# Optimization experiments

Hardware: AMD Instinct MI355X
Metric: run time of the kernel (lower is better)

The kernel has to match this reference:

```python
import jax, jax.numpy as jnp
import numpy as np

B, H, W, BLK = 32, 512, 512, 8
QF_MIN, QF_MAX, QF_BIAS = 2.0, 50.0, 0.0

_RGB2YCC = jnp.array([[0.299, 0.587, 0.114],
                      [-0.168736, -0.331264, 0.5],
                      [0.5, -0.418688, -0.081312]], jnp.float32)
_YCC_OFF = jnp.array([0.0, 128.0, 128.0], jnp.float32)

Y_QTB = jnp.array([16,11,10,16,24,40,51,61,12,12,14,19,26,58,60,55,14,13,16,24,40,57,69,56,
                   14,17,22,29,51,87,80,62,18,22,37,56,68,109,103,77,24,36,55,64,81,104,113,92,
                   49,64,78,87,103,121,120,101,72,92,95,98,112,100,103,99], jnp.float32).reshape(8, 8)
C_QTB = jnp.array([17,18,24,47,99,99,99,99,18,21,26,66,99,99,99,99,24,26,56,99,99,99,99,99,
                   47,66,99,99,99,99,99,99,99,99,99,99,99,99,99,99,99,99,99,99,99,99,99,99,
                   99,99,99,99,99,99,99,99,99,99,99,99,99,99,99,99], jnp.float32).reshape(8, 8)

# orthonormal 8x8 DCT-II matrix
_k = np.arange(8.0)[:, None]; _n = np.arange(8.0)[None, :]
_C = 0.5 * np.cos((2 * _n + 1) * _k * np.pi / 16.0)
_C[0] *= 1.0 / np.sqrt(2.0)
DCT_M = jnp.asarray(_C, jnp.float32)

# standard JPEG zig-zag raster order over the 64 coefficients of an 8x8 block
ZIGZAG = jnp.array([0,1,8,16,9,2,3,10,17,24,32,25,18,11,4,5,12,19,26,33,40,48,41,34,27,20,13,6,
                    7,14,21,28,35,42,49,56,57,50,43,36,29,22,15,23,30,37,44,51,58,59,52,45,38,31,
                    39,46,53,60,61,54,47,55,62,63], jnp.int32)


def hard_round(x):
    # straight-through round: forward = round(x), backward = identity
    return x + jax.lax.stop_gradient(jnp.round(x) - x)


def split_blocks(x):
    # [B,H,W] -> [B,H/8,W/8,8,8]
    b, h, w = x.shape
    return x.reshape(b, h // BLK, BLK, w // BLK, BLK).transpose(0, 1, 3, 2, 4)


def dct2d(x):
    # 2D DCT over the trailing 8x8 dims: C @ X @ C^T
    return jnp.einsum('ij,bnmjk,lk->bnmil', DCT_M, x, DCT_M)


def _norm01(e):
    mn = e.min(axis=(1, 2), keepdims=True)
    mx = e.max(axis=(1, 2), keepdims=True)
    return (e - mn) / (mx - mn + 1e-6)


def _ac_energy(d):
    # per-block log AC energy, shape [B,h8,w8]
    return jnp.log1p(jnp.sum(d * d, axis=(-2, -1)) - d[..., 0, 0] ** 2 + 1e-6)


def _forward(rgb):
    ycbcr = hard_round(jnp.einsum('bhwc,kc->bhwk', rgb, _RGB2YCC) + _YCC_OFF) - 128.0
    y_d = dct2d(split_blocks(ycbcr[..., 0]))
    cb_d = dct2d(split_blocks(ycbcr[..., 1]))
    cr_d = dct2d(split_blocks(ycbcr[..., 2]))

    # QFMapGenerator (default): per-block AC-energy rank in [0,1], upsampled to pixels
    rank = jnp.stack([_norm01(_ac_energy(y_d)),
                      _norm01(0.5 * (_ac_energy(cb_d) + _ac_energy(cr_d)))], axis=-1)  # [B,h8,w8,2]
    rank_px = jnp.repeat(jnp.repeat(rank, BLK, axis=1), BLK, axis=2)  # [B,H,W,2]

    # RankToQF
    enc_qf = jnp.clip(hard_round(QF_MIN + rank_px * (QF_MAX - QF_MIN) + QF_BIAS), QF_MIN, QF_MAX)
    y_qf_min = enc_qf[..., 0].min(axis=(1, 2), keepdims=True)
    y_qf_max = enc_qf[..., 0].max(axis=(1, 2), keepdims=True)
    c_qf_min = enc_qf[..., 1].min(axis=(1, 2), keepdims=True)
    c_qf_max = enc_qf[..., 1].max(axis=(1, 2), keepdims=True)

    # QFToScale: standard JPEG QF -> scale factor
    enc_scale = hard_round(jnp.where(enc_qf < 50.0, 5000.0 / enc_qf, 200.0 - 2.0 * enc_qf)) / 100.0

    sy = split_blocks(enc_scale[..., 0])  # [B,h8,w8,8,8]
    sc = split_blocks(enc_scale[..., 1])
    yq = hard_round(y_d / (sy * Y_QTB))
    cbq = hard_round(cb_d / (sc * C_QTB))
    crq = hard_round(cr_d / (sc * C_QTB))
    qdct = jnp.stack([yq, cbq, crq], axis=1)  # [B,3,h8,w8,8,8]

    nb = (H // BLK) * (W // BLK)
    flat = qdct.reshape(B, 3, nb, 64)
    # delta encode along the block axis
    delta = jnp.concatenate([flat[:, :, :1], flat[:, :, 1:] - flat[:, :, :-1]], axis=2)
    # zig-zag raster scan of the 64 coefficients
    zz = delta[..., ZIGZAG]
    blocks = jnp.log(jnp.abs(zz) + 1.0) / jnp.log(2.0)
    blocks = blocks.reshape(-1, 64)
    return qdct, blocks, enc_qf, enc_scale, y_qf_min, y_qf_max, c_qf_min, c_qf_max


def setup_inputs() -> dict:
    key = jax.random.key(0)
    rgb = jax.random.uniform(key, (B, H, W, 3), jnp.float32) * 255.0
    return {"rgb": rgb}


def reference(rgb):
    return _forward(rgb)
```

## Files before the change

kernel.cpp:

```cpp
#include <hip/hip_runtime.h>
#include <math.h>

#define BB 32
#define HH 512
#define WW 512
#define NB 4096
#define QD 25165824
#define PP 16777216
#define TAILOFF (2 * (size_t)QD + 2 * (size_t)PP)

__constant__ int c_zz[64] = {
    0,1,8,16,9,2,3,10,17,24,32,25,18,11,4,5,12,19,26,33,40,48,41,34,27,20,13,6,
    7,14,21,28,35,42,49,56,57,50,43,36,29,22,15,23,30,37,44,51,58,59,52,45,38,31,
    39,46,53,60,61,54,47,55,62,63};

struct QArg { float Cf[64]; double rqY[64]; double rqC[64]; };

__device__ __forceinline__ double qf_from_rank(double r) {
    double q = rint(2.0 + r * 48.0 + 0.0);
    return fmin(fmax(q, 2.0), 50.0);
}
__device__ __forceinline__ double scale_from_qf(double qf) {
    double s = (qf < 50.0) ? (5000.0 / qf) : (200.0 - 2.0 * qf);
    return rint(s) / 100.0;
}

__device__ __forceinline__ void ycc16(const float* __restrict__ src, int p0,
                                      int* y, int* cb, int* cr) {
    float px[48];
    const float4* s4 = (const float4*)(src + (size_t)p0 * 3);
    #pragma unroll
    for (int k = 0; k < 12; ++k) ((float4*)px)[k] = s4[k];
    #pragma unroll
    for (int k = 0; k < 16; ++k) {
        double R = px[3 * k], G = px[3 * k + 1], Bv = px[3 * k + 2];
        y[k]  = (int)(rint(R * (double)0.299f     + G * (double)0.587f     + Bv * (double)0.114f)             - 128.0);
        cb[k] = (int)(rint(R * (double)-0.168736f + G * (double)-0.331264f + Bv * (double)0.5f       + 128.0) - 128.0);
        cr[k] = (int)(rint(R * (double)0.5f       + G * (double)-0.418688f + Bv * (double)-0.081312f + 128.0) - 128.0);
    }
}

__global__ __launch_bounds__(256, 4) void k_energy(const float* __restrict__ rgb,
                                                   short* __restrict__ planes,
                                                   double* __restrict__ ey,
                                                   double* __restrict__ ec) {
    __shared__ int4 part[3][8][32];
    __shared__ double ecomb[2][64];
    int b = blockIdx.x >> 6, i = blockIdx.x & 63, t = threadIdx.x;
    const float* src = rgb + (size_t)(b * HH + i * 8) * WW * 3;
    {
        int y[16], cb[16], cr[16];
        ycc16(src, t * 16, y, cb, cr);
        int s[3][2] = {{0,0},{0,0},{0,0}}, s2[3][2] = {{0,0},{0,0},{0,0}};
        alignas(16) short yb[16], cbb[16], crb[16];
        #pragma unroll
        for (int k = 0; k < 16; ++k) {
            int h = k >> 3;
            s[0][h] += y[k];  s2[0][h] += y[k] * y[k];
            s[1][h] += cb[k]; s2[1][h] += cb[k] * cb[k];
            s[2][h] += cr[k]; s2[2][h] += cr[k] * cr[k];
            yb[k] = (short)y[k]; cbb[k] = (short)cb[k]; crb[k] = (short)cr[k];
        }
        size_t soff = (size_t)i * 4096 + (size_t)t * 16;
        short* d0 = planes + (((size_t)(b * 3 + 0)) << 18) + soff;
        short* d1 = planes + (((size_t)(b * 3 + 1)) << 18) + soff;
        short* d2 = planes + (((size_t)(b * 3 + 2)) << 18) + soff;
        ((int4*)d0)[0] = ((int4*)yb)[0];  ((int4*)d0)[1] = ((int4*)yb)[1];
        ((int4*)d1)[0] = ((int4*)cbb)[0]; ((int4*)d1)[1] = ((int4*)cbb)[1];
        ((int4*)d2)[0] = ((int4*)crb)[0]; ((int4*)d2)[1] = ((int4*)crb)[1];
        int r0 = t >> 5, c = t & 31;
        #pragma unroll
        for (int ch = 0; ch < 3; ++ch)
            part[ch][r0][c] = make_int4(s[ch][0], s2[ch][0], s[ch][1], s2[ch][1]);
    }
    __syncthreads();
    int ch = t >> 6, j = t & 63;
    if (ch < 3) {
        int S = 0, S2 = 0;
        #pragma unroll
        for (int r = 0; r < 8; ++r) {
            const int2* p = (const int2*)&part[ch][r][j >> 1];
            int2 v = p[j & 1];
            S += v.x; S2 += v.y;
        }
        double e = log1p((double)S2 - (double)S * (double)S * (1.0 / 64.0) + 1e-6);
        if (ch == 0) ey[b * NB + i * 64 + j] = e;
        else ecomb[ch - 1][j] = e;
    }
    __syncthreads();
    if (t < 64) ec[b * NB + i * 64 + t] = 0.5 * (ecomb[0][t] + ecomb[1][t]);
}

__global__ __launch_bounds__(256) void k_minmax(const double* __restrict__ ey,
                                                const double* __restrict__ ec,
                                                double* __restrict__ mm,
                                                float* __restrict__ out_tail) {
    __shared__ double s0[256], s1[256], s2[256], s3[256];
    int b = blockIdx.x, tid = threadIdx.x;
    double mny = 1e300, mxy = -1e300, mnc = 1e300, mxc = -1e300;
    for (int n = tid; n < NB; n += 256) {
        double vy = ey[b * NB + n], vc = ec[b * NB + n];
        mny = fmin(mny, vy); mxy = fmax(mxy, vy);
        mnc = fmin(mnc, vc); mxc = fmax(mxc, vc);
    }
    s0[tid] = mny; s1[tid] = mxy; s2[tid] = mnc; s3[tid] = mxc;
    __syncthreads();
    for (int off = 128; off > 0; off >>= 1) {
        if (tid < off) {
            s0[tid] = fmin(s0[tid], s0[tid + off]);
            s1[tid] = fmax(s1[tid], s1[tid + off]);
            s2[tid] = fmin(s2[tid], s2[tid + off]);
            s3[tid] = fmax(s3[tid], s3[tid + off]);
        }
        __syncthreads();
    }
    if (tid == 0) {
        mm[b] = s0[0]; mm[32 + b] = s1[0]; mm[64 + b] = s2[0]; mm[96 + b] = s3[0];
        double ry = (s1[0] - s0[0]) / (s1[0] - s0[0] + 1e-6);
        double rc = (s3[0] - s2[0]) / (s3[0] - s2[0] + 1e-6);
        out_tail[b]      = (float)qf_from_rank(0.0);
        out_tail[32 + b] = (float)qf_from_rank(ry);
        out_tail[64 + b] = (float)qf_from_rank(0.0);
        out_tail[96 + b] = (float)qf_from_rank(rc);
    }
}

__global__ __launch_bounds__(256, 4) void k_quant(const short* __restrict__ planes,
                                                  QArg A,
                                                  const double* __restrict__ ey,
                                                  const double* __restrict__ ec,
                                                  const double* __restrict__ mm,
                                                  float* __restrict__ out) {
    __shared__ __align__(16) char lds[27136];
    short* sqA = (short*)lds;
    float4* qsc = (float4*)(lds + 26112);

    int b = blockIdx.x >> 6, i = blockIdx.x & 63, t = threadIdx.x;
    int ch = t >> 6, j = t & 63;
    float U[8][8];
    double qy = 0, qc = 0, sy = 1, sc = 1;
    if (ch < 3) {
        int gt = b * NB + i * 64 + j;
        double eyv = ey[gt], ecv = ec[gt];
        double mny = mm[b], mxy = mm[32 + b], mnc = mm[64 + b], mxc = mm[96 + b];
        double ry = (eyv - mny) / (mxy - mny + 1e-6);
        double rc = (ecv - mnc) / (mxc - mnc + 1e-6);
        qy = qf_from_rank(ry); qc = qf_from_rank(rc);
        sy = scale_from_qf(qy); sc = scale_from_qf(qc);
        const short* pl = planes + (((size_t)(b * 3 + ch)) << 18)
                        + (size_t)i * 4096 + (size_t)j * 8;
        #pragma unroll
        for (int r = 0; r < 8; ++r) {
            alignas(16) short xs[8];
            *(int4*)xs = *(const int4*)(pl + (size_t)r * 512);
            float xr[8];
            #pragma unroll
            for (int s = 0; s < 8; ++s) xr[s] = (float)xs[s];
            #pragma unroll
            for (int v = 0; v < 8; ++v) {
                float u = 0.0f;
                #pragma unroll
                for (int s = 0; s < 8; ++s) u += xr[s] * A.Cf[v * 8 + s];
                U[r][v] = u;
            }
        }
        if (ch == 0) qsc[j] = make_float4((float)qy, (float)qc, (float)sy, (float)sc);
        double rinv = 1.0 / ((ch == 0) ? sy : sc);
        const double* rqt = (ch == 0) ? A.rqY : A.rqC;
        int row = (ch * 64 + j) * 68;
        #pragma unroll
        for (int u = 0; u < 8; ++u) {
            alignas(8) short srow[8];
            #pragma unroll
            for (int v = 0; v < 8; ++v) {
                float dq = (float)rint([&]{
                    float d = 0.0f;
                    #pragma unroll
                    for (int r = 0; r < 8; ++r) d += A.Cf[u * 8 + r] * U[r][v];
                    return (double)d * (rqt[u * 8 + v] * rinv);
                }());
                srow[v] = (short)(int)dq;
            }
            ((long long*)&sqA[row + u * 8])[0] = ((long long*)srow)[0];
            ((long long*)&sqA[row + u * 8 + 4])[0] = ((long long*)srow)[1];
        }
    }
    __syncthreads();

    size_t obase = ((size_t)b * 3 * NB + (size_t)i * 64) * 64;
    int k4 = (t & 15) * 4;
    #pragma unroll
    for (int it = 0; it < 12; ++it) {
        int m = it * 256 + t;
        int mch = m >> 10, f = m & 1023;
        int mj = f >> 4;
        alignas(8) short s4[4];
        *(long long*)s4 = *(const long long*)&sqA[(mch * 64 + mj) * 68 + k4];
        float4 v = make_float4((float)s4[0], (float)s4[1], (float)s4[2], (float)s4[3]);
        *(float4*)(out + obase + (size_t)mch * NB * 64 + (size_t)mj * 64 + k4) = v;
    }
    int zk0 = c_zz[k4], zk1 = c_zz[k4 + 1], zk2 = c_zz[k4 + 2], zk3 = c_zz[k4 + 3];
    #pragma unroll
    for (int it = 0; it < 12; ++it) {
        int m = it * 256 + t;
        int mch = m >> 10, f = m & 1023;
        int mj = f >> 4;
        int rowc = (mch * 64 + mj) * 68;
        int rowp = rowc - (mj ? 68 : 0);
        float d0 = (float)(sqA[rowc + zk0] - sqA[rowp + zk0]);
        float d1 = (float)(sqA[rowc + zk1] - sqA[rowp + zk1]);
        float d2 = (float)(sqA[rowc + zk2] - sqA[rowp + zk2]);
        float d3 = (float)(sqA[rowc + zk3] - sqA[rowp + zk3]);
        float4 v = make_float4(log2f(fabsf(d0) + 1.0f),
                               log2f(fabsf(d1) + 1.0f),
                               log2f(fabsf(d2) + 1.0f),
                               log2f(fabsf(d3) + 1.0f));
        *(float4*)(out + QD + obase + (size_t)mch * NB * 64 + (size_t)mj * 64 + k4) = v;
    }
    {
        float4 qs = qsc[t >> 2];
        float4 qv = make_float4(qs.x, qs.y, qs.x, qs.y);
        float4 sv = make_float4(qs.z, qs.w, qs.z, qs.w);
        float2* mq = (float2*)(out + 2 * (size_t)QD);
        float2* ms = (float2*)(out + 2 * (size_t)QD + PP);
        #pragma unroll
        for (int rr = 0; rr < 8; ++rr) {
            size_t P = ((size_t)(b * HH + i * 8 + rr)) * WW;
            ((float4*)(mq + P))[t] = qv;
            ((float4*)(ms + P))[t] = sv;
        }
    }
}

__global__ __launch_bounds__(256) void k_fix(const float* __restrict__ q,
                                             float* __restrict__ ob) {
    int idx = blockIdx.x * 256 + threadIdx.x;
    int rid = idx >> 6, k = idx & 63;
    int bch = rid >> 6;
    int i = rid & 63;
    size_t base = ((size_t)bch * NB + (size_t)i * 64) * 64;
    int zk = c_zz[k];
    float cur = q[base + zk];
    float prv = (i > 0) ? q[base - 64 + zk] : 0.0f;
    ob[base + k] = log2f(fabsf(cur - prv) + 1.0f);
}

extern "C" void kernel_launch(void* const* d_in, const int* in_sizes, int n_in,
                              void* d_out, int out_size, void* d_ws, size_t ws_size,
                              hipStream_t stream) {
    const float* rgb = (const float*)d_in[0];
    float* out = (float*)d_out;
    double* ws = (double*)d_ws;
    double* ey = ws;
    double* ec = ws + (size_t)BB * NB;
    double* mm = ws + 2 * (size_t)BB * NB;
    short* planes = (short*)(ws + 2 * (size_t)BB * NB + 128);

    static const double YQ[64] = {
        16,11,10,16,24,40,51,61, 12,12,14,19,26,58,60,55, 14,13,16,24,40,57,69,56,
        14,17,22,29,51,87,80,62, 18,22,37,56,68,109,103,77, 24,36,55,64,81,104,113,92,
        49,64,78,87,103,121,120,101, 72,92,95,98,112,100,103,99};
    static const double CQ[64] = {
        17,18,24,47,99,99,99,99, 18,21,26,66,99,99,99,99, 24,26,56,99,99,99,99,99,
        47,66,99,99,99,99,99,99, 99,99,99,99,99,99,99,99, 99,99,99,99,99,99,99,99,
        99,99,99,99,99,99,99,99, 99,99,99,99,99,99,99,99};

    QArg qa;
    for (int k = 0; k < 8; ++k)
        for (int n = 0; n < 8; ++n) {
            double v = 0.5 * cos((2.0 * n + 1.0) * (double)k * M_PI / 16.0);
            if (k == 0) v *= 0.70710678118654752440;
            qa.Cf[k * 8 + n] = (float)v;
        }
    for (int k = 0; k < 64; ++k) { qa.rqY[k] = 1.0 / YQ[k]; qa.rqC[k] = 1.0 / CQ[k]; }

    dim3 blk(256);
    k_energy<<<BB * 64, blk, 0, stream>>>(rgb, planes, ey, ec);
    k_minmax<<<BB, blk, 0, stream>>>(ey, ec, mm, out + TAILOFF);
    k_quant<<<BB * 64, blk, 0, stream>>>(planes, qa, ey, ec, mm, out);
    k_fix<<<(BB * 3 * 64 * 64) / 256, blk, 0, stream>>>(out, out + QD);
}
```

Baseline: 435.3 us.

## Fuse min/max reduction and cross-row delta fixup into quantization kernel

Removes the separate per-image min/max kernel: every quant block now redundantly reduces the image's 4096 energy values itself. It also drops the fixup kernel, which re-read the quantized output to redo the delta at row boundaries. Three extra threads now recompute the last block of the previous row into shared memory so the delta can be finished in-block. This cuts two launches and a large global read/write pass, at the cost of redundant reduction reads (64 blocks per image) and extra DCT work for three threads.

```diff
diff --git a/kernel.cpp b/kernel.cpp
--- a/kernel.cpp
+++ b/kernel.cpp
@@ -91,64 +91,71 @@
     if (t < 64) ec[b * NB + i * 64 + t] = 0.5 * (ecomb[0][t] + ecomb[1][t]);
 }
 
-__global__ __launch_bounds__(256) void k_minmax(const double* __restrict__ ey,
-                                                const double* __restrict__ ec,
-                                                double* __restrict__ mm,
-                                                float* __restrict__ out_tail) {
-    __shared__ double s0[256], s1[256], s2[256], s3[256];
-    int b = blockIdx.x, tid = threadIdx.x;
-    double mny = 1e300, mxy = -1e300, mnc = 1e300, mxc = -1e300;
-    for (int n = tid; n < NB; n += 256) {
-        double vy = ey[b * NB + n], vc = ec[b * NB + n];
-        mny = fmin(mny, vy); mxy = fmax(mxy, vy);
-        mnc = fmin(mnc, vc); mxc = fmax(mxc, vc);
-    }
-    s0[tid] = mny; s1[tid] = mxy; s2[tid] = mnc; s3[tid] = mxc;
-    __syncthreads();
-    for (int off = 128; off > 0; off >>= 1) {
-        if (tid < off) {
-            s0[tid] = fmin(s0[tid], s0[tid + off]);
-            s1[tid] = fmax(s1[tid], s1[tid + off]);
-            s2[tid] = fmin(s2[tid], s2[tid + off]);
-            s3[tid] = fmax(s3[tid], s3[tid + off]);
-        }
-        __syncthreads();
-    }
-    if (tid == 0) {
-        mm[b] = s0[0]; mm[32 + b] = s1[0]; mm[64 + b] = s2[0]; mm[96 + b] = s3[0];
-        double ry = (s1[0] - s0[0]) / (s1[0] - s0[0] + 1e-6);
-        double rc = (s3[0] - s2[0]) / (s3[0] - s2[0] + 1e-6);
-        out_tail[b]      = (float)qf_from_rank(0.0);
-        out_tail[32 + b] = (float)qf_from_rank(ry);
-        out_tail[64 + b] = (float)qf_from_rank(0.0);
-        out_tail[96 + b] = (float)qf_from_rank(rc);
-    }
-}
-
 __global__ __launch_bounds__(256, 4) void k_quant(const short* __restrict__ planes,
                                                   QArg A,
                                                   const double* __restrict__ ey,
                                                   const double* __restrict__ ec,
-                                                  const double* __restrict__ mm,
                                                   float* __restrict__ out) {
-    __shared__ __align__(16) char lds[27136];
+    __shared__ __align__(16) char lds[27584];
     short* sqA = (short*)lds;
-    float4* qsc = (float4*)(lds + 26112);
+    float4* qsc = (float4*)(lds + 26560);
+    double* red = (double*)lds;
 
     int b = blockIdx.x >> 6, i = blockIdx.x & 63, t = threadIdx.x;
-    int ch = t >> 6, j = t & 63;
-    float U[8][8];
-    double qy = 0, qc = 0, sy = 1, sc = 1;
-    if (ch < 3) {
-        int gt = b * NB + i * 64 + j;
+
+    double mny = 1e300, mxy = -1e300, mnc = 1e300, mxc = -1e300;
+    const double* eyb = ey + (size_t)b * NB;
+    const double* ecb = ec + (size_t)b * NB;
+    for (int n = t; n < NB; n += 256) {
+        double vy = eyb[n], vc = ecb[n];
+        mny = fmin(mny, vy); mxy = fmax(mxy, vy);
+        mnc = fmin(mnc, vc); mxc = fmax(mxc, vc);
+    }
+    red[t] = mny; red[256 + t] = mxy; red[512 + t] = mnc; red[768 + t] = mxc;
+    __syncthreads();
+    for (int off = 128; off > 0; off >>= 1) {
+        if (t < off) {
+            red[t]       = fmin(red[t],       red[t + off]);
+            red[256 + t] = fmax(red[256 + t], red[256 + t + off]);
+            red[512 + t] = fmin(red[512 + t], red[512 + t + off]);
+            red[768 + t] = fmax(red[768 + t], red[768 + t + off]);
+        }
+        __syncthreads();
+    }
+    mny = red[0]; mxy = red[256]; mnc = red[512]; mxc = red[768];
+    __syncthreads();
+
+    if (i == 0 && t == 0) {
+        double ry = (mxy - mny) / (mxy - mny + 1e-6);
+        double rc = (mxc - mnc) / (mxc - mnc + 1e-6);
+        float* tail = out + TAILOFF;
+        tail[b]      = (float)qf_from_rank(0.0);
+        tail[32 + b] = (float)qf_from_rank(ry);
+        tail[64 + b] = (float)qf_from_rank(0.0);
+        tail[96 + b] = (float)qf_from_rank(rc);
+    }
+
+    int ch = 0, j = 0, ii = i, row = 0;
+    bool act = false, zero = false;
+    if (t < 192)      { ch = t >> 6;  j = t & 63; row = (ch * 64 + j) * 68; act = true; }
+    else if (t < 195) { ch = t - 192; j = 63; ii = i - 1; row = (192 + ch) * 68;
+                        act = true; zero = (i == 0); }
+
+    if (act && zero) {
+        #pragma unroll
+        for (int u = 0; u < 16; ++u) ((long long*)&sqA[row])[u] = 0LL;
+    }
+    if (act && !zero) {
+        int gt = b * NB + ii * 64 + j;
         double eyv = ey[gt], ecv = ec[gt];
-        double mny = mm[b], mxy = mm[32 + b], mnc = mm[64 + b], mxc = mm[96 + b];
         double ry = (eyv - mny) / (mxy - mny + 1e-6);
         double rc = (ecv - mnc) / (mxc - mnc + 1e-6);
-        qy = qf_from_rank(ry); qc = qf_from_rank(rc);
-        sy = scale_from_qf(qy); sc = scale_from_qf(qc);
+        double qy = qf_from_rank(ry), qc = qf_from_rank(rc);
+        double sy = scale_from_qf(qy), sc = scale_from_qf(qc);
+        if (t < 64) qsc[j] = make_float4((float)qy, (float)qc, (float)sy, (float)sc);
         const short* pl = planes + (((size_t)(b * 3 + ch)) << 18)
-                        + (size_t)i * 4096 + (size_t)j * 8;
+                        + (size_t)ii * 4096 + (size_t)j * 8;
+        float U[8][8];
         #pragma unroll
         for (int r = 0; r < 8; ++r) {
             alignas(16) short xs[8];
@@ -164,10 +171,8 @@
                 U[r][v] = u;
             }
         }
-        if (ch == 0) qsc[j] = make_float4((float)qy, (float)qc, (float)sy, (float)sc);
         double rinv = 1.0 / ((ch == 0) ? sy : sc);
         const double* rqt = (ch == 0) ? A.rqY : A.rqC;
-        int row = (ch * 64 + j) * 68;
         #pragma unroll
         for (int u = 0; u < 8; ++u) {
             alignas(8) short srow[8];
@@ -206,7 +211,7 @@
         int mch = m >> 10, f = m & 1023;
         int mj = f >> 4;
         int rowc = (mch * 64 + mj) * 68;
-        int rowp = rowc - (mj ? 68 : 0);
+        int rowp = mj ? (rowc - 68) : (192 + mch) * 68;
         float d0 = (float)(sqA[rowc + zk0] - sqA[rowp + zk0]);
         float d1 = (float)(sqA[rowc + zk1] - sqA[rowp + zk1]);
         float d2 = (float)(sqA[rowc + zk2] - sqA[rowp + zk2]);
@@ -232,19 +237,6 @@
     }
 }
 
-__global__ __launch_bounds__(256) void k_fix(const float* __restrict__ q,
-                                             float* __restrict__ ob) {
-    int idx = blockIdx.x * 256 + threadIdx.x;
-    int rid = idx >> 6, k = idx & 63;
-    int bch = rid >> 6;
-    int i = rid & 63;
-    size_t base = ((size_t)bch * NB + (size_t)i * 64) * 64;
-    int zk = c_zz[k];
-    float cur = q[base + zk];
-    float prv = (i > 0) ? q[base - 64 + zk] : 0.0f;
-    ob[base + k] = log2f(fabsf(cur - prv) + 1.0f);
-}
-
 extern "C" void kernel_launch(void* const* d_in, const int* in_sizes, int n_in,
                               void* d_out, int out_size, void* d_ws, size_t ws_size,
                               hipStream_t stream) {
@@ -253,8 +245,7 @@
     double* ws = (double*)d_ws;
     double* ey = ws;
     double* ec = ws + (size_t)BB * NB;
-    double* mm = ws + 2 * (size_t)BB * NB;
-    short* planes = (short*)(ws + 2 * (size_t)BB * NB + 128);
+    short* planes = (short*)(ws + 2 * (size_t)BB * NB);
 
     static const double YQ[64] = {
         16,11,10,16,24,40,51,61, 12,12,14,19,26,58,60,55, 14,13,16,24,40,57,69,56,
@@ -276,7 +267,5 @@
 
     dim3 blk(256);
     k_energy<<<BB * 64, blk, 0, stream>>>(rgb, planes, ey, ec);
-    k_minmax<<<BB, blk, 0, stream>>>(ey, ec, mm, out + TAILOFF);
-    k_quant<<<BB * 64, blk, 0, stream>>>(planes, qa, ey, ec, mm, out);
-    k_fix<<<(BB * 3 * 64 * 64) / 256, blk, 0, stream>>>(out, out + QD);
-}
+    k_quant<<<BB * 64, blk, 0, stream>>>(planes, qa, ey, ec, out);
+}
```

After: 445.0 us. 1.02x slower.

## Store YCbCr planes as int8 and fold boundary delta fix into quant kernel

Applied to the files above, without the earlier changes.

The intermediate YCbCr planes are stored as signed 8-bit values instead of 16-bit shorts, halving the bytes written by the energy kernel and read by the quant kernel. The separate k_fix launch, which recomputed zig-zag deltas for the first block of each block-row, is removed. Instead, three extra threads in k_quant recompute the quantized last block of the previous row into LDS so the delta for j=0 is correct in place. This adds redundant DCT work for one block per channel per workgroup and depends on every rounded YCbCr value fitting in int8.

```diff
diff --git a/kernel.cpp b/kernel.cpp
--- a/kernel.cpp
+++ b/kernel.cpp
@@ -41,7 +41,7 @@
 }
 
 __global__ __launch_bounds__(256, 4) void k_energy(const float* __restrict__ rgb,
-                                                   short* __restrict__ planes,
+                                                   signed char* __restrict__ planes,
                                                    double* __restrict__ ey,
                                                    double* __restrict__ ec) {
     __shared__ int4 part[3][8][32];
@@ -52,22 +52,22 @@
         int y[16], cb[16], cr[16];
         ycc16(src, t * 16, y, cb, cr);
         int s[3][2] = {{0,0},{0,0},{0,0}}, s2[3][2] = {{0,0},{0,0},{0,0}};
-        alignas(16) short yb[16], cbb[16], crb[16];
+        alignas(16) signed char yb[16], cbb[16], crb[16];
         #pragma unroll
         for (int k = 0; k < 16; ++k) {
             int h = k >> 3;
             s[0][h] += y[k];  s2[0][h] += y[k] * y[k];
             s[1][h] += cb[k]; s2[1][h] += cb[k] * cb[k];
             s[2][h] += cr[k]; s2[2][h] += cr[k] * cr[k];
-            yb[k] = (short)y[k]; cbb[k] = (short)cb[k]; crb[k] = (short)cr[k];
+            yb[k] = (signed char)y[k]; cbb[k] = (signed char)cb[k]; crb[k] = (signed char)cr[k];
         }
         size_t soff = (size_t)i * 4096 + (size_t)t * 16;
-        short* d0 = planes + (((size_t)(b * 3 + 0)) << 18) + soff;
-        short* d1 = planes + (((size_t)(b * 3 + 1)) << 18) + soff;
-        short* d2 = planes + (((size_t)(b * 3 + 2)) << 18) + soff;
-        ((int4*)d0)[0] = ((int4*)yb)[0];  ((int4*)d0)[1] = ((int4*)yb)[1];
-        ((int4*)d1)[0] = ((int4*)cbb)[0]; ((int4*)d1)[1] = ((int4*)cbb)[1];
-        ((int4*)d2)[0] = ((int4*)crb)[0]; ((int4*)d2)[1] = ((int4*)crb)[1];
+        signed char* d0 = planes + (((size_t)(b * 3 + 0)) << 18) + soff;
+        signed char* d1 = planes + (((size_t)(b * 3 + 1)) << 18) + soff;
+        signed char* d2 = planes + (((size_t)(b * 3 + 2)) << 18) + soff;
+        *(int4*)d0 = *(int4*)yb;
+        *(int4*)d1 = *(int4*)cbb;
+        *(int4*)d2 = *(int4*)crb;
         int r0 = t >> 5, c = t & 31;
         #pragma unroll
         for (int ch = 0; ch < 3; ++ch)
@@ -125,34 +125,44 @@
     }
 }
 
-__global__ __launch_bounds__(256, 4) void k_quant(const short* __restrict__ planes,
+__global__ __launch_bounds__(256, 4) void k_quant(const signed char* __restrict__ planes,
                                                   QArg A,
                                                   const double* __restrict__ ey,
                                                   const double* __restrict__ ec,
                                                   const double* __restrict__ mm,
                                                   float* __restrict__ out) {
-    __shared__ __align__(16) char lds[27136];
+    __shared__ __align__(16) char lds[27584];
     short* sqA = (short*)lds;
-    float4* qsc = (float4*)(lds + 26112);
+    float4* qsc = (float4*)(lds + 26560);
 
     int b = blockIdx.x >> 6, i = blockIdx.x & 63, t = threadIdx.x;
-    int ch = t >> 6, j = t & 63;
-    float U[8][8];
-    double qy = 0, qc = 0, sy = 1, sc = 1;
-    if (ch < 3) {
-        int gt = b * NB + i * 64 + j;
+
+    int ch = 0, j = 0, ii = i, row = 0;
+    bool act = false, zero = false;
+    if (t < 192)      { ch = t >> 6;  j = t & 63; row = (ch * 64 + j) * 68; act = true; }
+    else if (t < 195) { ch = t - 192; j = 63; ii = i - 1; row = (192 + ch) * 68;
+                        act = true; zero = (i == 0); }
+
+    if (act && zero) {
+        #pragma unroll
+        for (int u = 0; u < 16; ++u) ((long long*)&sqA[row])[u] = 0LL;
+    }
+    if (act && !zero) {
+        int gt = b * NB + ii * 64 + j;
         double eyv = ey[gt], ecv = ec[gt];
         double mny = mm[b], mxy = mm[32 + b], mnc = mm[64 + b], mxc = mm[96 + b];
         double ry = (eyv - mny) / (mxy - mny + 1e-6);
         double rc = (ecv - mnc) / (mxc - mnc + 1e-6);
-        qy = qf_from_rank(ry); qc = qf_from_rank(rc);
-        sy = scale_from_qf(qy); sc = scale_from_qf(qc);
-        const short* pl = planes + (((size_t)(b * 3 + ch)) << 18)
-                        + (size_t)i * 4096 + (size_t)j * 8;
+        double qy = qf_from_rank(ry), qc = qf_from_rank(rc);
+        double sy = scale_from_qf(qy), sc = scale_from_qf(qc);
+        if (t < 64) qsc[j] = make_float4((float)qy, (float)qc, (float)sy, (float)sc);
+        const signed char* pl = planes + (((size_t)(b * 3 + ch)) << 18)
+                              + (size_t)ii * 4096 + (size_t)j * 8;
+        float U[8][8];
         #pragma unroll
         for (int r = 0; r < 8; ++r) {
-            alignas(16) short xs[8];
-            *(int4*)xs = *(const int4*)(pl + (size_t)r * 512);
+            alignas(8) signed char xs[8];
+            *(long long*)xs = *(const long long*)(pl + (size_t)r * 512);
             float xr[8];
             #pragma unroll
             for (int s = 0; s < 8; ++s) xr[s] = (float)xs[s];
@@ -164,10 +174,8 @@
                 U[r][v] = u;
             }
         }
-        if (ch == 0) qsc[j] = make_float4((float)qy, (float)qc, (float)sy, (float)sc);
         double rinv = 1.0 / ((ch == 0) ? sy : sc);
         const double* rqt = (ch == 0) ? A.rqY : A.rqC;
-        int row = (ch * 64 + j) * 68;
         #pragma unroll
         for (int u = 0; u < 8; ++u) {
             alignas(8) short srow[8];
@@ -206,7 +214,7 @@
         int mch = m >> 10, f = m & 1023;
         int mj = f >> 4;
         int rowc = (mch * 64 + mj) * 68;
-        int rowp = rowc - (mj ? 68 : 0);
+        int rowp = mj ? (rowc - 68) : (192 + mch) * 68;
         float d0 = (float)(sqA[rowc + zk0] - sqA[rowp + zk0]);
         float d1 = (float)(sqA[rowc + zk1] - sqA[rowp + zk1]);
         float d2 = (float)(sqA[rowc + zk2] - sqA[rowp + zk2]);
@@ -232,19 +240,6 @@
     }
 }
 
-__global__ __launch_bounds__(256) void k_fix(const float* __restrict__ q,
-                                             float* __restrict__ ob) {
-    int idx = blockIdx.x * 256 + threadIdx.x;
-    int rid = idx >> 6, k = idx & 63;
-    int bch = rid >> 6;
-    int i = rid & 63;
-    size_t base = ((size_t)bch * NB + (size_t)i * 64) * 64;
-    int zk = c_zz[k];
-    float cur = q[base + zk];
-    float prv = (i > 0) ? q[base - 64 + zk] : 0.0f;
-    ob[base + k] = log2f(fabsf(cur - prv) + 1.0f);
-}
-
 extern "C" void kernel_launch(void* const* d_in, const int* in_sizes, int n_in,
                               void* d_out, int out_size, void* d_ws, size_t ws_size,
                               hipStream_t stream) {
@@ -254,7 +249,7 @@
     double* ey = ws;
     double* ec = ws + (size_t)BB * NB;
     double* mm = ws + 2 * (size_t)BB * NB;
-    short* planes = (short*)(ws + 2 * (size_t)BB * NB + 128);
+    signed char* planes = (signed char*)(ws + 2 * (size_t)BB * NB + 128);
 
     static const double YQ[64] = {
         16,11,10,16,24,40,51,61, 12,12,14,19,26,58,60,55, 14,13,16,24,40,57,69,56,
@@ -278,5 +273,4 @@
     k_energy<<<BB * 64, blk, 0, stream>>>(rgb, planes, ey, ec);
     k_minmax<<<BB, blk, 0, stream>>>(ey, ec, mm, out + TAILOFF);
     k_quant<<<BB * 64, blk, 0, stream>>>(planes, qa, ey, ec, mm, out);
-    k_fix<<<(BB * 3 * 64 * 64) / 256, blk, 0, stream>>>(out, out + QD);
-}
+}
```

New measurement: 428.0 us. No clear change (-1.7%).
